# Performance work log

Hardware: AMD Instinct MI355X
Metric: run time of the kernel (lower is better)

## Reference

```python
import jax, jax.numpy as jnp
import numpy as np

N_BINS = 64
SIGMA_SCALE = 0.5
_LAB_RANGES = {'L': (0.0, 100.0), 'a': (-128.0, 127.0), 'b': (-128.0, 127.0)}


def _channel_params(vmin, vmax, n_bins=N_BINS, sigma_scale=SIGMA_SCALE):
    delta = (vmax - vmin) / n_bins
    centers = jnp.linspace(vmin + delta / 2, vmax - delta / 2, n_bins, dtype=jnp.float32)
    sigma = jnp.float32(delta * sigma_scale)
    return centers, sigma


def rgb_to_lab(rgb):
    # rgb: (B, 3, H, W) in [0, 1] sRGB
    thr = 0.04045
    lin = jnp.where(rgb > thr, jnp.power((rgb + 0.055) / 1.055, 2.4), rgb / 12.92)
    r, g, b = lin[:, 0], lin[:, 1], lin[:, 2]
    # sRGB -> XYZ (D65)
    x = 0.412453 * r + 0.357580 * g + 0.180423 * b
    y = 0.212671 * r + 0.715160 * g + 0.072169 * b
    z = 0.019334 * r + 0.119193 * g + 0.950227 * b
    xn, zn = 0.950456, 1.088754  # D65 white (Y normalized to 1)
    x = x / xn
    z = z / zn
    eps = 0.008856
    def f(t):
        return jnp.where(t > eps, jnp.cbrt(t), 7.787 * t + 16.0 / 116.0)
    fx, fy, fz = f(x), f(y), f(z)
    L = 116.0 * fy - 16.0
    a = 500.0 * (fx - fy)
    bb = 200.0 * (fy - fz)
    return jnp.stack([L, a, bb], axis=1)  # (B, 3, H, W)


def setup_inputs() -> dict:
    key = jax.random.key(0)
    img = jax.random.uniform(key, (16, 3, 512, 512), dtype=jnp.float32)
    return {"img": img}


def reference(img) -> jnp.ndarray:
    B = img.shape[0]
    img_lab = rgb_to_lab(img)  # (B, 3, H, W)
    parts = []
    for c_idx, name in enumerate(['L', 'a', 'b']):
        centers, sigma = _channel_params(*_LAB_RANGES[name])
        pixels = img_lab[:, c_idx].reshape(B, -1)  # (B, HW)
        diff = pixels[:, :, None] - centers[None, None, :]  # (B, HW, n_bins)
        weights = jnp.exp(-(diff ** 2) / (2.0 * sigma ** 2))
        hist_unnorm = weights.sum(axis=1)  # (B, n_bins)
        hist = hist_unnorm / (hist_unnorm.sum(axis=-1, keepdims=True) + 1e-8)
        parts.append(hist)
    return jnp.concatenate(parts, axis=1)  # (B, 192)
```

## Files before the change

kernel.cpp:

```cpp
#include <hip/hip_runtime.h>
#include <cmath>

#define HW (512*512)
#define NSUB 2048
#define THREADS1 1024
#define BLKS_PER_IMG 32
#define PART_WORDS (3 * NSUB / 2)

__device__ __forceinline__ float fexp2(float x) { return __builtin_amdgcn_exp2f(x); }
__device__ __forceinline__ float flog2(float x) { return __builtin_amdgcn_logf(x); }

__global__ __launch_bounds__(THREADS1) void count_kernel(const float* __restrict__ img,
                                                         unsigned* __restrict__ part) {
    __shared__ unsigned sh[2][3 * NSUB];
    const int tid = threadIdx.x;
    unsigned* flat = &sh[0][0];
    for (int i = tid; i < 2 * 3 * NSUB; i += THREADS1) flat[i] = 0u;
    __syncthreads();

    unsigned* h = sh[(tid >> 6) & 1];

    const int b  = blockIdx.y;
    const int bx = blockIdx.x;
    const float* base = img + (size_t)b * 3u * HW;

    const int stride = BLKS_PER_IMG * THREADS1 * 4;
    for (int p = (bx * THREADS1 + tid) * 4; p < HW; p += stride) {
        float4 r4 = *reinterpret_cast<const float4*>(base + p);
        float4 g4 = *reinterpret_cast<const float4*>(base + p + HW);
        float4 b4 = *reinterpret_cast<const float4*>(base + p + 2 * HW);
        float rr[4] = {r4.x, r4.y, r4.z, r4.w};
        float gg[4] = {g4.x, g4.y, g4.z, g4.w};
        float bl[4] = {b4.x, b4.y, b4.z, b4.w};

        #pragma unroll
        for (int k = 0; k < 4; ++k) {
            float lr = (rr[k] > 0.04045f) ? fexp2(2.4f * flog2((rr[k] + 0.055f) * (1.0f / 1.055f))) : rr[k] * (1.0f / 12.92f);
            float lg = (gg[k] > 0.04045f) ? fexp2(2.4f * flog2((gg[k] + 0.055f) * (1.0f / 1.055f))) : gg[k] * (1.0f / 12.92f);
            float lb = (bl[k] > 0.04045f) ? fexp2(2.4f * flog2((bl[k] + 0.055f) * (1.0f / 1.055f))) : bl[k] * (1.0f / 12.92f);

            float x = 0.4339530f * lr + 0.3762197f * lg + 0.1898288f * lb;
            float y = 0.2126710f * lr + 0.7151600f * lg + 0.0721690f * lb;
            float z = 0.0177578f * lr + 0.1094766f * lg + 0.8727661f * lb;

            float fx = (x > 0.008856f) ? fexp2(flog2(x) * (1.0f/3.0f)) : 7.787f * x + 16.0f/116.0f;
            float fy = (y > 0.008856f) ? fexp2(flog2(y) * (1.0f/3.0f)) : 7.787f * y + 16.0f/116.0f;
            float fz = (z > 0.008856f) ? fexp2(flog2(z) * (1.0f/3.0f)) : 7.787f * z + 16.0f/116.0f;

            int iL = (int)(2375.68f    * fy - 327.68f);
            int iA = (int)(4015.6863f  * (fx - fy) + 1028.01569f);
            int iB = (int)(1606.27451f * (fy - fz) + 1028.01569f);

            atomicAdd(&h[iL], 1u);
            atomicAdd(&h[NSUB + iA], 1u);
            atomicAdd(&h[2 * NSUB + iB], 1u);
        }
    }
    __syncthreads();

    unsigned* dst = part + (size_t)(b * BLKS_PER_IMG + bx) * PART_WORDS;
    for (int i = tid; i < PART_WORDS; i += THREADS1) {
        unsigned s0 = sh[0][2 * i]     + sh[1][2 * i];
        unsigned s1 = sh[0][2 * i + 1] + sh[1][2 * i + 1];
        dst[i] = s0 | (s1 << 16);
    }
}

__global__ __launch_bounds__(1024) void conv_norm_kernel(const unsigned* __restrict__ part,
                                                         float* __restrict__ out) {
    __shared__ float sub[NSUB];
    __shared__ float hb[64];
    const int img = blockIdx.x / 3;
    const int ch  = blockIdx.x % 3;
    const int t   = threadIdx.x;

    const unsigned* p0 = part + (size_t)img * BLKS_PER_IMG * PART_WORDS
                              + (size_t)ch * (NSUB / 2) + t;
    unsigned s0 = 0, s1 = 0;
    #pragma unroll
    for (int k = 0; k < BLKS_PER_IMG; ++k) {
        unsigned v = p0[(size_t)k * PART_WORDS];
        s0 += v & 0xFFFFu;
        s1 += v >> 16;
    }
    sub[2 * t]     = (float)s0;
    sub[2 * t + 1] = (float)s1;
    __syncthreads();

    const int j = t >> 4;
    const int q = t & 15;
    const float C = 2.8853901f;
    const float jf = (float)j + 0.5f - (0.5f / 32.0f);
    const int s_lo = 32 * j - 86;
    float acc = 0.0f;
    #pragma unroll
    for (int i = 0; i < 13; ++i) {
        int s = s_lo + q + 16 * i;
        if (s < s_lo + 204 && (unsigned)s < (unsigned)NSUB) {
            float d = (float)s * (1.0f / 32.0f) - jf;
            acc += sub[s] * fexp2(-C * d * d);
        }
    }
    acc += __shfl_xor(acc, 1, 64);
    acc += __shfl_xor(acc, 2, 64);
    acc += __shfl_xor(acc, 4, 64);
    acc += __shfl_xor(acc, 8, 64);
    if (q == 0) hb[j] = acc;
    __syncthreads();

    if (t < 64) {
        float v = hb[t];
        float s = v;
        #pragma unroll
        for (int off = 32; off >= 1; off >>= 1) s += __shfl_down(s, off, 64);
        s = __shfl(s, 0, 64);
        out[img * 192 + ch * 64 + t] = v / (s + 1e-8f);
    }
}

extern "C" void kernel_launch(void* const* d_in, const int* in_sizes, int n_in,
                              void* d_out, int out_size, void* d_ws, size_t ws_size,
                              hipStream_t stream) {
    const float* img = (const float*)d_in[0];
    float* out     = (float*)d_out;
    unsigned* part = (unsigned*)d_ws;

    const int B = in_sizes[0] / (3 * HW);

    count_kernel<<<dim3(BLKS_PER_IMG, B), THREADS1, 0, stream>>>(img, part);
    conv_norm_kernel<<<B * 3, 1024, 0, stream>>>(part, out);
}
```

Measured before the change: 87.19 us.

## Fuse count and conv-normalize kernels via last-block-done atomic counter

Merges the second kernel into the counting kernel. Each block publishes its partial histogram, bumps a per-image atomic counter, and the last block to finish for an image reduces all partials, applies the Gaussian smoothing for all three channels, and normalizes. This removes one kernel launch and the gap between the two kernels. In exchange it adds a memset launch for the counters, and the tail work for each image now runs on a single block instead of three.

Measured after the change: 260.6 us. +198.8%, slower.

```diff
diff --git a/kernel.cpp b/kernel.cpp
--- a/kernel.cpp
+++ b/kernel.cpp
@@ -10,9 +10,13 @@
 __device__ __forceinline__ float fexp2(float x) { return __builtin_amdgcn_exp2f(x); }
 __device__ __forceinline__ float flog2(float x) { return __builtin_amdgcn_logf(x); }
 
-__global__ __launch_bounds__(THREADS1) void count_kernel(const float* __restrict__ img,
-                                                         unsigned* __restrict__ part) {
+__global__ __launch_bounds__(THREADS1) void count_fused(const float* __restrict__ img,
+                                                        unsigned* __restrict__ part,
+                                                        unsigned* __restrict__ done,
+                                                        float* __restrict__ out) {
     __shared__ unsigned sh[2][3 * NSUB];
+    __shared__ float hb[3][64];
+    __shared__ int lastFlag;
     const int tid = threadIdx.x;
     unsigned* flat = &sh[0][0];
     for (int i = tid; i < 2 * 3 * NSUB; i += THREADS1) flat[i] = 0u;
@@ -64,57 +68,69 @@
         unsigned s1 = sh[0][2 * i + 1] + sh[1][2 * i + 1];
         dst[i] = s0 | (s1 << 16);
     }
-}
+    __threadfence();
+    __syncthreads();
+    if (tid == 0) {
+        unsigned old = __hip_atomic_fetch_add(&done[b], 1u, __ATOMIC_ACQ_REL,
+                                              __HIP_MEMORY_SCOPE_AGENT);
+        lastFlag = (old == BLKS_PER_IMG - 1);
+    }
+    __syncthreads();
+    if (!lastFlag) return;
 
-__global__ __launch_bounds__(1024) void conv_norm_kernel(const unsigned* __restrict__ part,
-                                                         float* __restrict__ out) {
-    __shared__ float sub[NSUB];
-    __shared__ float hb[64];
-    const int img = blockIdx.x / 3;
-    const int ch  = blockIdx.x % 3;
-    const int t   = threadIdx.x;
-
-    const unsigned* p0 = part + (size_t)img * BLKS_PER_IMG * PART_WORDS
-                              + (size_t)ch * (NSUB / 2) + t;
-    unsigned s0 = 0, s1 = 0;
-    #pragma unroll
-    for (int k = 0; k < BLKS_PER_IMG; ++k) {
-        unsigned v = p0[(size_t)k * PART_WORDS];
-        s0 += v & 0xFFFFu;
-        s1 += v >> 16;
+    float* sub3 = reinterpret_cast<float*>(&sh[0][0]);
+    const unsigned long long* pimg = reinterpret_cast<const unsigned long long*>(
+        part + (size_t)b * BLKS_PER_IMG * PART_WORDS);
+    for (int w = tid; w < PART_WORDS / 2; w += THREADS1) {
+        unsigned s0 = 0, s1 = 0, s2 = 0, s3 = 0;
+        #pragma unroll
+        for (int k = 0; k < BLKS_PER_IMG; ++k) {
+            unsigned long long v = __hip_atomic_load(
+                &pimg[(size_t)k * (PART_WORDS / 2) + w],
+                __ATOMIC_RELAXED, __HIP_MEMORY_SCOPE_AGENT);
+            unsigned lo = (unsigned)v, hi = (unsigned)(v >> 32);
+            s0 += lo & 0xFFFFu; s1 += lo >> 16;
+            s2 += hi & 0xFFFFu; s3 += hi >> 16;
+        }
+        sub3[4 * w]     = (float)s0;
+        sub3[4 * w + 1] = (float)s1;
+        sub3[4 * w + 2] = (float)s2;
+        sub3[4 * w + 3] = (float)s3;
     }
-    sub[2 * t]     = (float)s0;
-    sub[2 * t + 1] = (float)s1;
     __syncthreads();
 
-    const int j = t >> 4;
-    const int q = t & 15;
+    const int j = tid >> 4;
+    const int q = tid & 15;
     const float C = 2.8853901f;
     const float jf = (float)j + 0.5f - (0.5f / 32.0f);
     const int s_lo = 32 * j - 86;
-    float acc = 0.0f;
     #pragma unroll
-    for (int i = 0; i < 13; ++i) {
-        int s = s_lo + q + 16 * i;
-        if (s < s_lo + 204 && (unsigned)s < (unsigned)NSUB) {
-            float d = (float)s * (1.0f / 32.0f) - jf;
-            acc += sub[s] * fexp2(-C * d * d);
+    for (int ch = 0; ch < 3; ++ch) {
+        float acc = 0.0f;
+        #pragma unroll
+        for (int i = 0; i < 13; ++i) {
+            int s = s_lo + q + 16 * i;
+            if (q + 16 * i < 204 && (unsigned)s < (unsigned)NSUB) {
+                float d = (float)s * (1.0f / 32.0f) - jf;
+                acc += sub3[ch * NSUB + s] * fexp2(-C * d * d);
+            }
         }
+        acc += __shfl_xor(acc, 1, 64);
+        acc += __shfl_xor(acc, 2, 64);
+        acc += __shfl_xor(acc, 4, 64);
+        acc += __shfl_xor(acc, 8, 64);
+        if (q == 0) hb[ch][j] = acc;
     }
-    acc += __shfl_xor(acc, 1, 64);
-    acc += __shfl_xor(acc, 2, 64);
-    acc += __shfl_xor(acc, 4, 64);
-    acc += __shfl_xor(acc, 8, 64);
-    if (q == 0) hb[j] = acc;
     __syncthreads();
 
-    if (t < 64) {
-        float v = hb[t];
+    if (tid < 192) {
+        const int ch = tid >> 6, bin = tid & 63;
+        float v = hb[ch][bin];
         float s = v;
         #pragma unroll
         for (int off = 32; off >= 1; off >>= 1) s += __shfl_down(s, off, 64);
         s = __shfl(s, 0, 64);
-        out[img * 192 + ch * 64 + t] = v / (s + 1e-8f);
+        out[b * 192 + ch * 64 + bin] = v / (s + 1e-8f);
     }
 }
 
@@ -126,7 +142,8 @@
     unsigned* part = (unsigned*)d_ws;
 
     const int B = in_sizes[0] / (3 * HW);
+    unsigned* done = part + (size_t)B * BLKS_PER_IMG * PART_WORDS;
 
-    count_kernel<<<dim3(BLKS_PER_IMG, B), THREADS1, 0, stream>>>(img, part);
-    conv_norm_kernel<<<B * 3, 1024, 0, stream>>>(part, out);
+    hipMemsetAsync(done, 0, B * sizeof(unsigned), stream);
+    count_fused<<<dim3(BLKS_PER_IMG, B), THREADS1, 0, stream>>>(img, part, done, out);
 }
```

## Fuse Gaussian smoothing into count kernel and reduce per-block 192-bin partials

Applied to the files above, without the earlier changes.

Each counting block now converts its own fine sub-bin histogram to float and applies the Gaussian bin smoothing itself, relying on the convolution being linear. It then writes 192 float partials instead of 3072 packed count words. A light finalize kernel sums the 32 block partials per image and normalises each channel. The pixel loop is also flattened so each thread handles exactly 8 pixels. This shrinks the workspace traffic and removes most of the second kernel, at the cost of repeating the smoothing math in every block.

Measured after the change: 89.44 us. 1.03x slower.

```diff
diff --git a/kernel.cpp b/kernel.cpp
--- a/kernel.cpp
+++ b/kernel.cpp
@@ -5,14 +5,14 @@
 #define NSUB 2048
 #define THREADS1 1024
 #define BLKS_PER_IMG 32
-#define PART_WORDS (3 * NSUB / 2)
 
 __device__ __forceinline__ float fexp2(float x) { return __builtin_amdgcn_exp2f(x); }
 __device__ __forceinline__ float flog2(float x) { return __builtin_amdgcn_logf(x); }
 
-__global__ __launch_bounds__(THREADS1) void count_kernel(const float* __restrict__ img,
-                                                         unsigned* __restrict__ part) {
+__global__ __launch_bounds__(THREADS1) void count_conv_kernel(const float* __restrict__ img,
+                                                              float* __restrict__ part) {
     __shared__ unsigned sh[2][3 * NSUB];
+    __shared__ float hb[3][64];
     const int tid = threadIdx.x;
     unsigned* flat = &sh[0][0];
     for (int i = tid; i < 2 * 3 * NSUB; i += THREADS1) flat[i] = 0u;
@@ -24,98 +24,92 @@
     const int bx = blockIdx.x;
     const float* base = img + (size_t)b * 3u * HW;
 
-    const int stride = BLKS_PER_IMG * THREADS1 * 4;
-    for (int p = (bx * THREADS1 + tid) * 4; p < HW; p += stride) {
-        float4 r4 = *reinterpret_cast<const float4*>(base + p);
-        float4 g4 = *reinterpret_cast<const float4*>(base + p + HW);
-        float4 b4 = *reinterpret_cast<const float4*>(base + p + 2 * HW);
-        float rr[4] = {r4.x, r4.y, r4.z, r4.w};
-        float gg[4] = {g4.x, g4.y, g4.z, g4.w};
-        float bl[4] = {b4.x, b4.y, b4.z, b4.w};
+    const int p = (bx * THREADS1 + tid) * 8;
+    float4 r4a = *reinterpret_cast<const float4*>(base + p);
+    float4 r4b = *reinterpret_cast<const float4*>(base + p + 4);
+    float4 g4a = *reinterpret_cast<const float4*>(base + p + HW);
+    float4 g4b = *reinterpret_cast<const float4*>(base + p + HW + 4);
+    float4 b4a = *reinterpret_cast<const float4*>(base + p + 2 * HW);
+    float4 b4b = *reinterpret_cast<const float4*>(base + p + 2 * HW + 4);
+    float rr[8] = {r4a.x, r4a.y, r4a.z, r4a.w, r4b.x, r4b.y, r4b.z, r4b.w};
+    float gg[8] = {g4a.x, g4a.y, g4a.z, g4a.w, g4b.x, g4b.y, g4b.z, g4b.w};
+    float bl[8] = {b4a.x, b4a.y, b4a.z, b4a.w, b4b.x, b4b.y, b4b.z, b4b.w};
 
-        #pragma unroll
-        for (int k = 0; k < 4; ++k) {
-            float lr = (rr[k] > 0.04045f) ? fexp2(2.4f * flog2((rr[k] + 0.055f) * (1.0f / 1.055f))) : rr[k] * (1.0f / 12.92f);
-            float lg = (gg[k] > 0.04045f) ? fexp2(2.4f * flog2((gg[k] + 0.055f) * (1.0f / 1.055f))) : gg[k] * (1.0f / 12.92f);
-            float lb = (bl[k] > 0.04045f) ? fexp2(2.4f * flog2((bl[k] + 0.055f) * (1.0f / 1.055f))) : bl[k] * (1.0f / 12.92f);
+    #pragma unroll
+    for (int k = 0; k < 8; ++k) {
+        float lr = (rr[k] > 0.04045f) ? fexp2(2.4f * flog2((rr[k] + 0.055f) * (1.0f / 1.055f))) : rr[k] * (1.0f / 12.92f);
+        float lg = (gg[k] > 0.04045f) ? fexp2(2.4f * flog2((gg[k] + 0.055f) * (1.0f / 1.055f))) : gg[k] * (1.0f / 12.92f);
+        float lb = (bl[k] > 0.04045f) ? fexp2(2.4f * flog2((bl[k] + 0.055f) * (1.0f / 1.055f))) : bl[k] * (1.0f / 12.92f);
 
-            float x = 0.4339530f * lr + 0.3762197f * lg + 0.1898288f * lb;
-            float y = 0.2126710f * lr + 0.7151600f * lg + 0.0721690f * lb;
-            float z = 0.0177578f * lr + 0.1094766f * lg + 0.8727661f * lb;
+        float x = 0.4339530f * lr + 0.3762197f * lg + 0.1898288f * lb;
+        float y = 0.2126710f * lr + 0.7151600f * lg + 0.0721690f * lb;
+        float z = 0.0177578f * lr + 0.1094766f * lg + 0.8727661f * lb;
 
-            float fx = (x > 0.008856f) ? fexp2(flog2(x) * (1.0f/3.0f)) : 7.787f * x + 16.0f/116.0f;
-            float fy = (y > 0.008856f) ? fexp2(flog2(y) * (1.0f/3.0f)) : 7.787f * y + 16.0f/116.0f;
-            float fz = (z > 0.008856f) ? fexp2(flog2(z) * (1.0f/3.0f)) : 7.787f * z + 16.0f/116.0f;
+        float fx = (x > 0.008856f) ? fexp2(flog2(x) * (1.0f/3.0f)) : 7.787f * x + 16.0f/116.0f;
+        float fy = (y > 0.008856f) ? fexp2(flog2(y) * (1.0f/3.0f)) : 7.787f * y + 16.0f/116.0f;
+        float fz = (z > 0.008856f) ? fexp2(flog2(z) * (1.0f/3.0f)) : 7.787f * z + 16.0f/116.0f;
 
-            int iL = (int)(2375.68f    * fy - 327.68f);
-            int iA = (int)(4015.6863f  * (fx - fy) + 1028.01569f);
-            int iB = (int)(1606.27451f * (fy - fz) + 1028.01569f);
+        int iL = (int)(2375.68f    * fy - 327.68f);
+        int iA = (int)(4015.6863f  * (fx - fy) + 1028.01569f);
+        int iB = (int)(1606.27451f * (fy - fz) + 1028.01569f);
 
-            atomicAdd(&h[iL], 1u);
-            atomicAdd(&h[NSUB + iA], 1u);
-            atomicAdd(&h[2 * NSUB + iB], 1u);
-        }
+        atomicAdd(&h[iL], 1u);
+        atomicAdd(&h[NSUB + iA], 1u);
+        atomicAdd(&h[2 * NSUB + iB], 1u);
     }
     __syncthreads();
 
-    unsigned* dst = part + (size_t)(b * BLKS_PER_IMG + bx) * PART_WORDS;
-    for (int i = tid; i < PART_WORDS; i += THREADS1) {
-        unsigned s0 = sh[0][2 * i]     + sh[1][2 * i];
-        unsigned s1 = sh[0][2 * i + 1] + sh[1][2 * i + 1];
-        dst[i] = s0 | (s1 << 16);
+    float* subf = reinterpret_cast<float*>(&sh[0][0]);
+    for (int i = tid; i < 3 * NSUB; i += THREADS1) {
+        unsigned s = sh[0][i] + sh[1][i];
+        subf[i] = (float)s;
+    }
+    __syncthreads();
+
+    const int j = tid >> 4;
+    const int q = tid & 15;
+    const float C = 2.8853901f;
+    const float jf = (float)j + 0.5f - (0.5f / 32.0f);
+    const int s_lo = 32 * j - 86;
+    #pragma unroll
+    for (int ch = 0; ch < 3; ++ch) {
+        float acc = 0.0f;
+        #pragma unroll
+        for (int i = 0; i < 13; ++i) {
+            int off = q + 16 * i;
+            int s = s_lo + off;
+            if (off < 204 && (unsigned)s < (unsigned)NSUB) {
+                float d = (float)s * (1.0f / 32.0f) - jf;
+                acc += subf[ch * NSUB + s] * fexp2(-C * d * d);
+            }
+        }
+        acc += __shfl_xor(acc, 1, 64);
+        acc += __shfl_xor(acc, 2, 64);
+        acc += __shfl_xor(acc, 4, 64);
+        acc += __shfl_xor(acc, 8, 64);
+        if (q == 0) hb[ch][j] = acc;
+    }
+    __syncthreads();
+
+    if (tid < 192) {
+        float* dst = part + (size_t)(b * BLKS_PER_IMG + bx) * 192;
+        dst[tid] = (&hb[0][0])[tid];
     }
 }
 
-__global__ __launch_bounds__(1024) void conv_norm_kernel(const unsigned* __restrict__ part,
-                                                         float* __restrict__ out) {
-    __shared__ float sub[NSUB];
-    __shared__ float hb[64];
-    const int img = blockIdx.x / 3;
-    const int ch  = blockIdx.x % 3;
-    const int t   = threadIdx.x;
-
-    const unsigned* p0 = part + (size_t)img * BLKS_PER_IMG * PART_WORDS
-                              + (size_t)ch * (NSUB / 2) + t;
-    unsigned s0 = 0, s1 = 0;
+__global__ __launch_bounds__(192) void finalize_kernel(const float* __restrict__ part,
+                                                       float* __restrict__ out) {
+    const int b = blockIdx.x;
+    const int t = threadIdx.x;
+    const float* p0 = part + (size_t)b * BLKS_PER_IMG * 192 + t;
+    float v = 0.0f;
     #pragma unroll
-    for (int k = 0; k < BLKS_PER_IMG; ++k) {
-        unsigned v = p0[(size_t)k * PART_WORDS];
-        s0 += v & 0xFFFFu;
-        s1 += v >> 16;
-    }
-    sub[2 * t]     = (float)s0;
-    sub[2 * t + 1] = (float)s1;
-    __syncthreads();
-
-    const int j = t >> 4;
-    const int q = t & 15;
-    const float C = 2.8853901f;
-    const float jf = (float)j + 0.5f - (0.5f / 32.0f);
-    const int s_lo = 32 * j - 86;
-    float acc = 0.0f;
+    for (int k = 0; k < BLKS_PER_IMG; ++k) v += p0[k * 192];
+    float s = v;
     #pragma unroll
-    for (int i = 0; i < 13; ++i) {
-        int s = s_lo + q + 16 * i;
-        if (s < s_lo + 204 && (unsigned)s < (unsigned)NSUB) {
-            float d = (float)s * (1.0f / 32.0f) - jf;
-            acc += sub[s] * fexp2(-C * d * d);
-        }
-    }
-    acc += __shfl_xor(acc, 1, 64);
-    acc += __shfl_xor(acc, 2, 64);
-    acc += __shfl_xor(acc, 4, 64);
-    acc += __shfl_xor(acc, 8, 64);
-    if (q == 0) hb[j] = acc;
-    __syncthreads();
-
-    if (t < 64) {
-        float v = hb[t];
-        float s = v;
-        #pragma unroll
-        for (int off = 32; off >= 1; off >>= 1) s += __shfl_down(s, off, 64);
-        s = __shfl(s, 0, 64);
-        out[img * 192 + ch * 64 + t] = v / (s + 1e-8f);
-    }
+    for (int off = 32; off >= 1; off >>= 1) s += __shfl_down(s, off, 64);
+    s = __shfl(s, 0, 64);
+    out[b * 192 + t] = v / (s + 1e-8f);
 }
 
 extern "C" void kernel_launch(void* const* d_in, const int* in_sizes, int n_in,
@@ -123,10 +117,10 @@
                               hipStream_t stream) {
     const float* img = (const float*)d_in[0];
     float* out     = (float*)d_out;
-    unsigned* part = (unsigned*)d_ws;
+    float* part    = (float*)d_ws;
 
     const int B = in_sizes[0] / (3 * HW);
 
-    count_kernel<<<dim3(BLKS_PER_IMG, B), THREADS1, 0, stream>>>(img, part);
-    conv_norm_kernel<<<B * 3, 1024, 0, stream>>>(part, out);
+    count_conv_kernel<<<dim3(BLKS_PER_IMG, B), THREADS1, 0, stream>>>(img, part);
+    finalize_kernel<<<B, 192, 0, stream>>>(part, out);
 }
```

## Interleave LDS histogram copies per lane, unroll eight pixels, trim Gaussian window

Applied to the files above, without the earlier changes.

The two shared-memory histogram copies are now chosen by lane parity (tid&1) instead of by wave, and padded to an odd stride. The aim is to cut same-address LDS atomic contention within a wavefront and to spread bank accesses. Each thread now handles eight pixels in one pass with no loop, and zeroing uses 16-byte stores. The smoothing kernel narrows its Gaussian window from 204 to 160 sub-bins and rotates the start index per bin to spread LDS bank accesses. The narrower window slightly truncates the Gaussian tail, which risks a small accuracy change.

After: 87.44 us. About the same (+0.3%).

```diff
diff --git a/kernel.cpp b/kernel.cpp
--- a/kernel.cpp
+++ b/kernel.cpp
@@ -6,62 +6,67 @@
 #define THREADS1 1024
 #define BLKS_PER_IMG 32
 #define PART_WORDS (3 * NSUB / 2)
+#define TBL (3 * NSUB + 1)
 
 __device__ __forceinline__ float fexp2(float x) { return __builtin_amdgcn_exp2f(x); }
 __device__ __forceinline__ float flog2(float x) { return __builtin_amdgcn_logf(x); }
 
 __global__ __launch_bounds__(THREADS1) void count_kernel(const float* __restrict__ img,
                                                          unsigned* __restrict__ part) {
-    __shared__ unsigned sh[2][3 * NSUB];
+    __align__(16) __shared__ unsigned sh[2 * TBL + 2];
     const int tid = threadIdx.x;
-    unsigned* flat = &sh[0][0];
-    for (int i = tid; i < 2 * 3 * NSUB; i += THREADS1) flat[i] = 0u;
+    {
+        uint4* z = reinterpret_cast<uint4*>(sh);
+        const uint4 zero = {0u, 0u, 0u, 0u};
+        for (int i = tid; i < (2 * TBL + 2) / 4; i += THREADS1) z[i] = zero;
+    }
     __syncthreads();
 
-    unsigned* h = sh[(tid >> 6) & 1];
+    unsigned* h = sh + (tid & 1) * TBL;
 
     const int b  = blockIdx.y;
     const int bx = blockIdx.x;
     const float* base = img + (size_t)b * 3u * HW;
 
-    const int stride = BLKS_PER_IMG * THREADS1 * 4;
-    for (int p = (bx * THREADS1 + tid) * 4; p < HW; p += stride) {
-        float4 r4 = *reinterpret_cast<const float4*>(base + p);
-        float4 g4 = *reinterpret_cast<const float4*>(base + p + HW);
-        float4 b4 = *reinterpret_cast<const float4*>(base + p + 2 * HW);
-        float rr[4] = {r4.x, r4.y, r4.z, r4.w};
-        float gg[4] = {g4.x, g4.y, g4.z, g4.w};
-        float bl[4] = {b4.x, b4.y, b4.z, b4.w};
+    const int p = (bx * THREADS1 + tid) * 8;
+    float4 r4a = *reinterpret_cast<const float4*>(base + p);
+    float4 r4b = *reinterpret_cast<const float4*>(base + p + 4);
+    float4 g4a = *reinterpret_cast<const float4*>(base + p + HW);
+    float4 g4b = *reinterpret_cast<const float4*>(base + p + HW + 4);
+    float4 b4a = *reinterpret_cast<const float4*>(base + p + 2 * HW);
+    float4 b4b = *reinterpret_cast<const float4*>(base + p + 2 * HW + 4);
+    float rr[8] = {r4a.x, r4a.y, r4a.z, r4a.w, r4b.x, r4b.y, r4b.z, r4b.w};
+    float gg[8] = {g4a.x, g4a.y, g4a.z, g4a.w, g4b.x, g4b.y, g4b.z, g4b.w};
+    float bl[8] = {b4a.x, b4a.y, b4a.z, b4a.w, b4b.x, b4b.y, b4b.z, b4b.w};
 
-        #pragma unroll
-        for (int k = 0; k < 4; ++k) {
-            float lr = (rr[k] > 0.04045f) ? fexp2(2.4f * flog2((rr[k] + 0.055f) * (1.0f / 1.055f))) : rr[k] * (1.0f / 12.92f);
-            float lg = (gg[k] > 0.04045f) ? fexp2(2.4f * flog2((gg[k] + 0.055f) * (1.0f / 1.055f))) : gg[k] * (1.0f / 12.92f);
-            float lb = (bl[k] > 0.04045f) ? fexp2(2.4f * flog2((bl[k] + 0.055f) * (1.0f / 1.055f))) : bl[k] * (1.0f / 12.92f);
+    #pragma unroll
+    for (int k = 0; k < 8; ++k) {
+        float lr = (rr[k] > 0.04045f) ? fexp2(2.4f * flog2((rr[k] + 0.055f) * (1.0f / 1.055f))) : rr[k] * (1.0f / 12.92f);
+        float lg = (gg[k] > 0.04045f) ? fexp2(2.4f * flog2((gg[k] + 0.055f) * (1.0f / 1.055f))) : gg[k] * (1.0f / 12.92f);
+        float lb = (bl[k] > 0.04045f) ? fexp2(2.4f * flog2((bl[k] + 0.055f) * (1.0f / 1.055f))) : bl[k] * (1.0f / 12.92f);
 
-            float x = 0.4339530f * lr + 0.3762197f * lg + 0.1898288f * lb;
-            float y = 0.2126710f * lr + 0.7151600f * lg + 0.0721690f * lb;
-            float z = 0.0177578f * lr + 0.1094766f * lg + 0.8727661f * lb;
+        float x = 0.4339530f * lr + 0.3762197f * lg + 0.1898288f * lb;
+        float y = 0.2126710f * lr + 0.7151600f * lg + 0.0721690f * lb;
+        float z = 0.0177578f * lr + 0.1094766f * lg + 0.8727661f * lb;
 
-            float fx = (x > 0.008856f) ? fexp2(flog2(x) * (1.0f/3.0f)) : 7.787f * x + 16.0f/116.0f;
-            float fy = (y > 0.008856f) ? fexp2(flog2(y) * (1.0f/3.0f)) : 7.787f * y + 16.0f/116.0f;
-            float fz = (z > 0.008856f) ? fexp2(flog2(z) * (1.0f/3.0f)) : 7.787f * z + 16.0f/116.0f;
+        float fx = (x > 0.008856f) ? fexp2(flog2(x) * (1.0f/3.0f)) : 7.787f * x + 16.0f/116.0f;
+        float fy = (y > 0.008856f) ? fexp2(flog2(y) * (1.0f/3.0f)) : 7.787f * y + 16.0f/116.0f;
+        float fz = (z > 0.008856f) ? fexp2(flog2(z) * (1.0f/3.0f)) : 7.787f * z + 16.0f/116.0f;
 
-            int iL = (int)(2375.68f    * fy - 327.68f);
-            int iA = (int)(4015.6863f  * (fx - fy) + 1028.01569f);
-            int iB = (int)(1606.27451f * (fy - fz) + 1028.01569f);
+        int iL = (int)(2375.68f    * fy - 327.68f);
+        int iA = (int)(4015.6863f  * (fx - fy) + 1028.01569f);
+        int iB = (int)(1606.27451f * (fy - fz) + 1028.01569f);
 
-            atomicAdd(&h[iL], 1u);
-            atomicAdd(&h[NSUB + iA], 1u);
-            atomicAdd(&h[2 * NSUB + iB], 1u);
-        }
+        atomicAdd(&h[iL], 1u);
+        atomicAdd(&h[NSUB + iA], 1u);
+        atomicAdd(&h[2 * NSUB + iB], 1u);
     }
     __syncthreads();
 
     unsigned* dst = part + (size_t)(b * BLKS_PER_IMG + bx) * PART_WORDS;
     for (int i = tid; i < PART_WORDS; i += THREADS1) {
-        unsigned s0 = sh[0][2 * i]     + sh[1][2 * i];
-        unsigned s1 = sh[0][2 * i + 1] + sh[1][2 * i + 1];
+        unsigned s0 = sh[2 * i]     + sh[TBL + 2 * i];
+        unsigned s1 = sh[2 * i + 1] + sh[TBL + 2 * i + 1];
         dst[i] = s0 | (s1 << 16);
     }
 }
@@ -91,12 +96,13 @@
     const int q = t & 15;
     const float C = 2.8853901f;
     const float jf = (float)j + 0.5f - (0.5f / 32.0f);
-    const int s_lo = 32 * j - 86;
+    const int s_lo = 32 * j - 64;
     float acc = 0.0f;
     #pragma unroll
-    for (int i = 0; i < 13; ++i) {
-        int s = s_lo + q + 16 * i;
-        if (s < s_lo + 204 && (unsigned)s < (unsigned)NSUB) {
+    for (int i = 0; i < 10; ++i) {
+        int m = i + (j % 10); if (m >= 10) m -= 10;
+        int s = s_lo + q + 16 * m;
+        if ((unsigned)s < (unsigned)NSUB) {
             float d = (float)s * (1.0f / 32.0f) - jf;
             acc += sub[s] * fexp2(-C * d * d);
         }
```
